# Kernel optimization log

Measured on AMD Instinct MI355X. Metric: run time of the kernel, lower is better.

The kernel has to match this reference:

```python
import jax, jax.numpy as jnp
import numpy as np

N_GRAPHS = 200
NODES_PER_GRAPH = 500
N_NODES = N_GRAPHS * NODES_PER_GRAPH  # 100000
N_EDGES = 1_600_000
INPUT_DIM = 64
GCN_DIM = 128
SEQ_LEN = 20
LSTM_DIM = 128
OUTPUT_DIM = 1


def setup_inputs() -> dict:
    key = jax.random.key(0)
    ks = jax.random.split(key, 10)
    # edges constrained to stay inside each graph (block-diagonal adjacency)
    src = jax.random.randint(ks[0], (N_EDGES,), 0, N_NODES, dtype=jnp.int32)
    dst_local = jax.random.randint(ks[1], (N_EDGES,), 0, NODES_PER_GRAPH, dtype=jnp.int32)
    dst = (src // NODES_PER_GRAPH) * NODES_PER_GRAPH + dst_local
    graph_ids = jnp.arange(N_NODES, dtype=jnp.int32) // NODES_PER_GRAPH
    x = jax.random.normal(ks[2], (N_NODES, INPUT_DIM), dtype=jnp.float32)
    s = 0.05
    w_gcn = jax.random.normal(ks[3], (INPUT_DIM, GCN_DIM), dtype=jnp.float32) * s
    b_gcn = jnp.zeros((GCN_DIM,), dtype=jnp.float32)
    w_ih = jax.random.normal(ks[4], (4 * LSTM_DIM, GCN_DIM), dtype=jnp.float32) * s
    w_hh = jax.random.normal(ks[5], (4 * LSTM_DIM, LSTM_DIM), dtype=jnp.float32) * s
    b_ih = jax.random.normal(ks[6], (4 * LSTM_DIM,), dtype=jnp.float32) * s
    b_hh = jax.random.normal(ks[7], (4 * LSTM_DIM,), dtype=jnp.float32) * s
    w_fc = jax.random.normal(ks[8], (OUTPUT_DIM, LSTM_DIM), dtype=jnp.float32) * s
    b_fc = jnp.zeros((OUTPUT_DIM,), dtype=jnp.float32)
    return {"x": x, "src": src, "dst": dst, "graph_ids": graph_ids,
            "w_gcn": w_gcn, "b_gcn": b_gcn, "w_ih": w_ih, "w_hh": w_hh,
            "b_ih": b_ih, "b_hh": b_hh, "w_fc": w_fc, "b_fc": b_fc}


def reference(x, src, dst, graph_ids, w_gcn, b_gcn, w_ih, w_hh, b_ih, b_hh, w_fc, b_fc):
    ones_e = jnp.ones((src.shape[0],), dtype=x.dtype)
    # DGL GraphConv norm='both': D_out^{-1/2} on src side, D_in^{-1/2} on dst side,
    # degrees clamped to min 1 (allow_zero_in_degree=True)
    out_deg = jnp.clip(jax.ops.segment_sum(ones_e, src, num_segments=N_NODES), 1.0)
    in_deg = jnp.clip(jax.ops.segment_sum(ones_e, dst, num_segments=N_NODES), 1.0)
    h = x * (out_deg ** -0.5)[:, None]                               # [N, Din]
    agg = jax.ops.segment_sum(h[src], dst, num_segments=N_NODES)     # gather+scatter-add
    h = agg * (in_deg ** -0.5)[:, None]
    h = jnp.maximum(h @ w_gcn + b_gcn, 0.0)                           # [N, GCN_DIM], ReLU
    # dgl.mean_nodes: per-graph mean pool
    cnt = jax.ops.segment_sum(jnp.ones((N_NODES,), h.dtype), graph_ids, num_segments=N_GRAPHS)
    hg = jax.ops.segment_sum(h, graph_ids, num_segments=N_GRAPHS) / cnt[:, None]  # [T, D]
    # build_dataset: sliding windows of length SEQ_LEN over the graph time series
    B = N_GRAPHS - SEQ_LEN + 1
    idx = jnp.arange(B)[:, None] + jnp.arange(SEQ_LEN)[None, :]
    dat = hg[idx]                                                      # [B, L, D]
    # single-layer LSTM (PyTorch gate order i,f,g,o), zero initial state
    x_proj = jnp.einsum('bld,gd->blg', dat, w_ih) + b_ih               # [B, L, 4H]
    h0 = jnp.zeros((B, LSTM_DIM), dat.dtype)
    c0 = jnp.zeros((B, LSTM_DIM), dat.dtype)

    def step(carry, xt):
        hprev, cprev = carry
        gates = xt + hprev @ w_hh.T + b_hh
        i, f, g, o = jnp.split(gates, 4, axis=-1)
        c = jax.nn.sigmoid(f) * cprev + jax.nn.sigmoid(i) * jnp.tanh(g)
        hh = jax.nn.sigmoid(o) * jnp.tanh(c)
        return (hh, c), None

    (h_n, _), _ = jax.lax.scan(step, (h0, c0), jnp.swapaxes(x_proj, 0, 1))
    pred = h_n @ w_fc.T + b_fc                                         # [B, OUTPUT_DIM]
    return pred
```

## Files before the change

### kernel.cpp

```cpp
#include <hip/hip_runtime.h>
#include <hip/hip_bf16.h>

#define N_GRAPHS 200
#define NPG      500
#define NPGP     512
#define N_NODES_ 100000
#define N_EDGES_ 1600000
#define DIN      64
#define DG       128
#define SEQ      20
#define HL       128
#define G4       512
#define BWIN     (N_GRAPHS - SEQ + 1)
#define NPART    256
#define EPB      (N_EDGES_/NPART)
#define SLOTS    64
#define CAP      9216

typedef __attribute__((ext_vector_type(8))) short short8;
typedef __attribute__((ext_vector_type(4))) float float4v;
typedef __attribute__((ext_vector_type(2))) _Float16 half2v;

__device__ __forceinline__ float sigmoidf_(float v){ return 1.0f/(1.0f+__expf(-v)); }
__device__ __forceinline__ float tanhf_(float x){
  float e = __expf(2.0f*x);
  return 1.0f - 2.0f/(e + 1.0f);
}

__device__ __forceinline__ unsigned short f2bf(float f) {
  unsigned int u = __float_as_uint(f);
  u += 0x7fffu + ((u >> 16) & 1u);
  return (unsigned short)(u >> 16);
}

__device__ __forceinline__ float h2dot(half2v a, half2v b, float c) {
#if __has_builtin(__builtin_amdgcn_fdot2)
  return __builtin_amdgcn_fdot2(a, b, c, false);
#else
  return c + (float)a.x*(float)b.x + (float)a.y*(float)b.y;
#endif
}

__global__ __launch_bounds__(1024) void k_part(const int* __restrict__ src,
                                               const int* __restrict__ dst,
                                               const float* __restrict__ w_hh,
                                               int* __restrict__ gcount,
                                               int* __restrict__ part,
                                               int4* __restrict__ whh16) {
  __shared__ int cnt[N_GRAPHS];
  __shared__ int base[N_GRAPHS];
  __shared__ int buf[N_GRAPHS][SLOTS];
  int b = blockIdx.x, t = threadIdx.x;
  if (b < 8) {
    int i = b*1024 + t;
    int k4 = i >> 9, r = i & 511;
    const float4* wp = (const float4*)(w_hh + (size_t)r*HL + k4*8);
    float4 w0 = wp[0], w1 = wp[1];
    half2v p0 = {(_Float16)w0.x, (_Float16)w0.y};
    half2v p1 = {(_Float16)w0.z, (_Float16)w0.w};
    half2v p2 = {(_Float16)w1.x, (_Float16)w1.y};
    half2v p3 = {(_Float16)w1.z, (_Float16)w1.w};
    int4 pk;
    pk.x = __builtin_bit_cast(int, p0); pk.y = __builtin_bit_cast(int, p1);
    pk.z = __builtin_bit_cast(int, p2); pk.w = __builtin_bit_cast(int, p3);
    whh16[i] = pk;
  }
  if (t < N_GRAPHS) cnt[t] = 0;
  __syncthreads();
  int e0 = b*EPB;
  const int2* s2 = (const int2*)(src + e0);
  const int2* d2 = (const int2*)(dst + e0);
  for (int i = t; i < EPB/2; i += 1024) {
    int2 ss = s2[i], dd = d2[i];
    {
      int g = ss.x / NPG;
      int pk = ((ss.x - g*NPG) << 9) | (dd.x - g*NPG);
      int pos = atomicAdd(&cnt[g], 1);
      if (pos < SLOTS) buf[g][pos] = pk;
      else { int gp = atomicAdd(&gcount[g], 1); part[g*CAP + gp] = pk; }
    }
    {
      int g = ss.y / NPG;
      int pk = ((ss.y - g*NPG) << 9) | (dd.y - g*NPG);
      int pos = atomicAdd(&cnt[g], 1);
      if (pos < SLOTS) buf[g][pos] = pk;
      else { int gp = atomicAdd(&gcount[g], 1); part[g*CAP + gp] = pk; }
    }
  }
  __syncthreads();
  if (t < N_GRAPHS) base[t] = atomicAdd(&gcount[t], min(cnt[t], SLOTS));
  __syncthreads();
  int w = t >> 6, lane = t & 63;
  for (int g = w; g < N_GRAPHS; g += 16) {
    int n = min(cnt[g], SLOTS);
    if (lane < n) part[g*CAP + base[g] + lane] = buf[g][lane];
  }
}

__global__ __launch_bounds__(1024) void k_graph(
    const int* __restrict__ gcount, const int* __restrict__ part,
    const float* __restrict__ x,
    const float* __restrict__ w_gcn, const float* __restrict__ b_gcn,
    const float* __restrict__ w_ih,  const float* __restrict__ b_ih,
    float* __restrict__ proj) {
  __shared__ int meta[2048];
  __shared__ int wsum[8];
  __shared__ int qhead;
  __shared__ __align__(16) float hgS[DG];
  __shared__ unsigned short sorted[CAP];
  __shared__ __align__(16) int4 xs[4008];
  __shared__ __align__(16) int4 hpre[4096];
  int* indeg  = meta;
  int* outdeg = meta + 512;
  int* off    = meta + 1024;
  float* soS  = (float*)(meta + 1536);
  int g = blockIdx.x, t = threadIdx.x;
  int lane = t & 63, w = t >> 6;

  float4 wg[2];
  #pragma unroll
  for (int q = 0; q < 2; ++q) wg[q] = ((const float4*)w_gcn)[t + q*1024];

  meta[t] = 0; meta[t + 1024] = 0;
  __syncthreads();
  int nseg = gcount[g], seg0 = g*CAP;
  int pr[9];
  #pragma unroll
  for (int q = 0; q < 9; ++q) {
    int e = t + q*1024;
    pr[q] = (e < nseg) ? part[seg0 + e] : -1;
  }
  #pragma unroll
  for (int q = 0; q < 9; ++q) {
    int p = pr[q];
    if (p >= 0) {
      atomicAdd(&indeg[p & 511], 1);
      atomicAdd(&outdeg[p >> 9], 1);
    }
  }
  __syncthreads();
  int vscan = 0, scscan = 0;
  if (t < 512) {
    vscan = indeg[t]; scscan = vscan;
    #pragma unroll
    for (int o = 1; o < 64; o <<= 1) { int nn = __shfl_up(scscan, o); if (lane >= o) scscan += nn; }
    if (lane == 63) wsum[w] = scscan;
  }
  __syncthreads();
  if (t < 512) {
    int woff = 0;
    #pragma unroll
    for (int i = 0; i < 8; ++i) woff += (i < w) ? wsum[i] : 0;
    off[t] = woff + scscan - vscan;
    soS[t] = rsqrtf((float)max(outdeg[t], 1));
  }
  __syncthreads();
  const float4* xg = ((const float4*)x) + (size_t)g*8000;
  ushort4* xd = (ushort4*)xs;
  for (int i = t; i < 8000; i += 1024) {
    float4 vv = xg[i];
    float s2 = soS[i >> 4];
    ushort4 u;
    u.x = f2bf(vv.x*s2); u.y = f2bf(vv.y*s2); u.z = f2bf(vv.z*s2); u.w = f2bf(vv.w*s2);
    xd[i] = u;
  }
  if (t < 16) xd[8000 + t] = make_ushort4(0,0,0,0);
  #pragma unroll
  for (int q = 0; q < 9; ++q) {
    int p = pr[q];
    if (p >= 0) {
      int pos = atomicAdd(&off[p & 511], 1);
      sorted[pos] = (unsigned short)(p >> 9);
    }
  }
  if (t == 0) qhead = 128;
  __syncthreads();
  int g8 = lane >> 3, fl = lane & 7;
  int nl = w*8 + g8;
  while (nl < 512) {
    int4 outv = make_int4(0,0,0,0);
    if (nl < NPG) {
      int end = off[nl], dgr = indeg[nl], st = end - dgr;
      float aHi[4] = {0.f,0.f,0.f,0.f};
      float aLo[4] = {0.f,0.f,0.f,0.f};
      int ev = (fl < dgr) ? (int)sorted[st + fl] : 500;
      for (int c0 = 0; c0 < dgr; c0 += 8) {
        int nc = c0 + 8;
        int evn = (nc + fl < dgr) ? (int)sorted[st + nc + fl] : 500;
        #pragma unroll
        for (int j = 0; j < 8; ++j) {
          int se = __shfl(ev, (g8 << 3) + j);
          int4 vv = xs[(se << 3) + fl];
          aHi[0] += __uint_as_float((unsigned)vv.x & 0xffff0000u);
          aLo[0] += __uint_as_float((unsigned)vv.x << 16);
          aHi[1] += __uint_as_float((unsigned)vv.y & 0xffff0000u);
          aLo[1] += __uint_as_float((unsigned)vv.y << 16);
          aHi[2] += __uint_as_float((unsigned)vv.z & 0xffff0000u);
          aLo[2] += __uint_as_float((unsigned)vv.z << 16);
          aHi[3] += __uint_as_float((unsigned)vv.w & 0xffff0000u);
          aLo[3] += __uint_as_float((unsigned)vv.w << 16);
        }
        ev = evn;
      }
      float sn = rsqrtf((float)max(dgr, 1));
      outv.x = (int)(((unsigned)f2bf(aLo[0]*sn)) | ((unsigned)f2bf(aHi[0]*sn) << 16));
      outv.y = (int)(((unsigned)f2bf(aLo[1]*sn)) | ((unsigned)f2bf(aHi[1]*sn) << 16));
      outv.z = (int)(((unsigned)f2bf(aLo[2]*sn)) | ((unsigned)f2bf(aHi[2]*sn) << 16));
      outv.w = (int)(((unsigned)f2bf(aLo[3]*sn)) | ((unsigned)f2bf(aHi[3]*sn) << 16));
    }
    hpre[(nl << 3) + (fl ^ (nl & 7))] = outv;
    int nxt = 0;
    if (fl == 0) nxt = atomicAdd(&qhead, 1);
    nl = __shfl(nxt, (g8 << 3));
  }
  __syncthreads();
  unsigned short* wLds = (unsigned short*)sorted;
  #pragma unroll
  for (int q = 0; q < 2; ++q) {
    int i = t + q*1024;
    int k = i >> 5, c4 = (i & 31) << 2;
    int h = k >> 5, j = k & 7, lhi = ((k >> 3) & 3) << 4;
    float vvv[4] = {wg[q].x, wg[q].y, wg[q].z, wg[q].w};
    #pragma unroll
    for (int u = 0; u < 4; ++u) {
      int n = c4 + u;
      int idx = ((n >> 4)*2 + h)*64 + lhi + (n & 15);
      wLds[idx*8 + j] = f2bf(vvv[u]);
    }
  }
  __syncthreads();
  float* pS = (float*)meta;
  int quad = lane >> 4, l15 = lane & 15;
  float bcol[8];
  #pragma unroll
  for (int nt = 0; nt < 8; ++nt) bcol[nt] = b_gcn[nt*16 + l15];
  float psum[8] = {0.f,0.f,0.f,0.f,0.f,0.f,0.f,0.f};
  #pragma unroll
  for (int i = 0; i < 2; ++i) {
    int row0 = (w + 16*i) << 4;
    int r = row0 + l15;
    int4 a0i = hpre[(r << 3) + (quad ^ (r & 7))];
    int4 a1i = hpre[(r << 3) + ((quad + 4) ^ (r & 7))];
    short8 a0 = *(const short8*)&a0i;
    short8 a1 = *(const short8*)&a1i;
    #pragma unroll
    for (int nt = 0; nt < 8; ++nt) {
      short8 b0 = *((const short8*)&wLds[((nt*2+0)*64 + lane)*8]);
      short8 b1 = *((const short8*)&wLds[((nt*2+1)*64 + lane)*8]);
      float4v acc = {0.f, 0.f, 0.f, 0.f};
      acc = __builtin_amdgcn_mfma_f32_16x16x32_bf16(a0, b0, acc, 0, 0, 0);
      acc = __builtin_amdgcn_mfma_f32_16x16x32_bf16(a1, b1, acc, 0, 0, 0);
      #pragma unroll
      for (int r4 = 0; r4 < 4; ++r4) {
        int node = row0 + quad*4 + r4;
        float vvv = acc[r4] + bcol[nt];
        psum[nt] += (node < NPG) ? fmaxf(vvv, 0.f) : 0.f;
      }
    }
  }
  #pragma unroll
  for (int nt = 0; nt < 8; ++nt) {
    float vvv = psum[nt];
    vvv += __shfl_xor(vvv, 16);
    vvv += __shfl_xor(vvv, 32);
    if (lane < 16) pS[w*DG + nt*16 + lane] = vvv;
  }
  __syncthreads();
  if (t < DG) {
    float sum = 0.f;
    #pragma unroll
    for (int w16 = 0; w16 < 16; ++w16) sum += pS[w16*DG + t];
    hgS[t] = sum * (1.0f/NPG);
  }
  __syncthreads();
  {
    int r = t >> 1, half = t & 1;
    const float4* wr = (const float4*)(w_ih + (size_t)r*HL) + half*16;
    const float4* hv = (const float4*)hgS + half*16;
    float acc = half ? 0.f : b_ih[r];
    #pragma unroll
    for (int k4 = 0; k4 < 16; ++k4) {
      float4 w4 = wr[k4]; float4 h4 = hv[k4];
      acc += w4.x*h4.x + w4.y*h4.y + w4.z*h4.z + w4.w*h4.w;
    }
    acc += __shfl_xor(acc, 1);
    if (!half) proj[(size_t)g*G4 + r] = acc;
  }
}

__global__ __launch_bounds__(512) void k_lstm(const float* __restrict__ proj,
    const int4* __restrict__ whh16, const float* __restrict__ b_hh,
    const float* __restrict__ w_fc, const float* __restrict__ b_fc,
    float* __restrict__ out) {
  __shared__ float gS[G4];
  __shared__ __align__(16) int4 hPi[16];
  __shared__ float fcS[2];
  int b = blockIdx.x, t = threadIdx.x;
  float pj[SEQ];
  #pragma unroll
  for (int l = 0; l < SEQ; ++l) pj[l] = proj[(size_t)(b+l)*G4 + t];
  int4 W[16];
  #pragma unroll
  for (int k4 = 0; k4 < 16; ++k4) W[k4] = whh16[(k4 << 9) + t];
  if (t < 16) hPi[t] = make_int4(0,0,0,0);
  float bh = b_hh[t];
  float c = 0.f;
  __syncthreads();
  #pragma unroll
  for (int l = 0; l < SEQ; ++l) {
    float a0 = pj[l] + bh;
    float a1 = 0.f, a2 = 0.f, a3 = 0.f;
    #pragma unroll
    for (int k4 = 0; k4 < 16; k4 += 4) {
      int4 hv0 = hPi[k4+0]; int4 hv1 = hPi[k4+1];
      int4 hv2 = hPi[k4+2]; int4 hv3 = hPi[k4+3];
      a0 = h2dot(__builtin_bit_cast(half2v, W[k4+0].x), __builtin_bit_cast(half2v, hv0.x), a0);
      a0 = h2dot(__builtin_bit_cast(half2v, W[k4+0].y), __builtin_bit_cast(half2v, hv0.y), a0);
      a0 = h2dot(__builtin_bit_cast(half2v, W[k4+0].z), __builtin_bit_cast(half2v, hv0.z), a0);
      a0 = h2dot(__builtin_bit_cast(half2v, W[k4+0].w), __builtin_bit_cast(half2v, hv0.w), a0);
      a1 = h2dot(__builtin_bit_cast(half2v, W[k4+1].x), __builtin_bit_cast(half2v, hv1.x), a1);
      a1 = h2dot(__builtin_bit_cast(half2v, W[k4+1].y), __builtin_bit_cast(half2v, hv1.y), a1);
      a1 = h2dot(__builtin_bit_cast(half2v, W[k4+1].z), __builtin_bit_cast(half2v, hv1.z), a1);
      a1 = h2dot(__builtin_bit_cast(half2v, W[k4+1].w), __builtin_bit_cast(half2v, hv1.w), a1);
      a2 = h2dot(__builtin_bit_cast(half2v, W[k4+2].x), __builtin_bit_cast(half2v, hv2.x), a2);
      a2 = h2dot(__builtin_bit_cast(half2v, W[k4+2].y), __builtin_bit_cast(half2v, hv2.y), a2);
      a2 = h2dot(__builtin_bit_cast(half2v, W[k4+2].z), __builtin_bit_cast(half2v, hv2.z), a2);
      a2 = h2dot(__builtin_bit_cast(half2v, W[k4+2].w), __builtin_bit_cast(half2v, hv2.w), a2);
      a3 = h2dot(__builtin_bit_cast(half2v, W[k4+3].x), __builtin_bit_cast(half2v, hv3.x), a3);
      a3 = h2dot(__builtin_bit_cast(half2v, W[k4+3].y), __builtin_bit_cast(half2v, hv3.y), a3);
      a3 = h2dot(__builtin_bit_cast(half2v, W[k4+3].z), __builtin_bit_cast(half2v, hv3.z), a3);
      a3 = h2dot(__builtin_bit_cast(half2v, W[k4+3].w), __builtin_bit_cast(half2v, hv3.w), a3);
    }
    gS[t] = (a0 + a1) + (a2 + a3);
    __syncthreads();
    if (t < 128) {
      float iv = sigmoidf_(gS[t]);
      float fv = sigmoidf_(gS[HL + t]);
      float gv = tanhf_(gS[2*HL + t]);
      float ov = sigmoidf_(gS[3*HL + t]);
      c = fv*c + iv*gv;
      float h = ov * tanhf_(c);
      float hp2 = __shfl_xor(h, 1);
      if (!(t & 1)) {
        half2v hp = {(_Float16)h, (_Float16)hp2};
        ((int*)hPi)[t >> 1] = __builtin_bit_cast(int, hp);
      }
      if (l == SEQ-1) {
        float s = h * w_fc[t];
        #pragma unroll
        for (int o = 32; o > 0; o >>= 1) s += __shfl_down(s, o);
        if ((t & 63) == 0) fcS[t >> 6] = s;
      }
    }
    __syncthreads();
  }
  if (t == 0) out[b] = fcS[0] + fcS[1] + b_fc[0];
}

extern "C" void kernel_launch(void* const* d_in, const int* in_sizes, int n_in,
                              void* d_out, int out_size, void* d_ws, size_t ws_size,
                              hipStream_t stream) {
  const float* x     = (const float*)d_in[0];
  const int*   src   = (const int*)d_in[1];
  const int*   dst   = (const int*)d_in[2];
  const float* w_gcn = (const float*)d_in[4];
  const float* b_gcn = (const float*)d_in[5];
  const float* w_ih  = (const float*)d_in[6];
  const float* w_hh  = (const float*)d_in[7];
  const float* b_ih  = (const float*)d_in[8];
  const float* b_hh  = (const float*)d_in[9];
  const float* w_fc  = (const float*)d_in[10];
  const float* b_fc  = (const float*)d_in[11];
  float* out = (float*)d_out;

  char* ws = (char*)d_ws;
  size_t off = 0;
  auto alloc = [&](size_t bytes) -> void* {
    void* p = ws + off; off += (bytes + 255) & ~(size_t)255; return p;
  };
  int* gcount  = (int*)alloc((size_t)N_GRAPHS*4);
  int* part    = (int*)alloc((size_t)N_GRAPHS*CAP*4);
  int4* whh16  = (int4*)alloc((size_t)8192*16);
  float* proj  = (float*)alloc((size_t)N_GRAPHS*G4*4);
  (void)ws_size; (void)in_sizes; (void)n_in; (void)out_size;

  hipMemsetAsync(gcount, 0, (size_t)N_GRAPHS*4, stream);
  k_part<<<NPART, 1024, 0, stream>>>(src, dst, w_hh, gcount, part, whh16);
  k_graph<<<N_GRAPHS, 1024, 0, stream>>>(gcount, part, x, w_gcn, b_gcn, w_ih, b_ih, proj);
  k_lstm<<<BWIN, 512, 0, stream>>>(proj, whh16, b_hh, w_fc, b_fc, out);
}
```

Measured before the change: 154.5 us.

## Use fixed per-block edge cells, padded neighbor lists, and a shuffle-based LSTM step

```diff
diff --git a/kernel.cpp b/kernel.cpp
--- a/kernel.cpp
+++ b/kernel.cpp
@@ -3,7 +3,6 @@
 
 #define N_GRAPHS 200
 #define NPG      500
-#define NPGP     512
 #define N_NODES_ 100000
 #define N_EDGES_ 1600000
 #define DIN      64
@@ -14,11 +13,13 @@
 #define BWIN     (N_GRAPHS - SEQ + 1)
 #define NPART    256
 #define EPB      (N_EDGES_/NPART)
-#define SLOTS    64
-#define CAP      9216
+#define CELL     80
+#define CPG      (NPART*CELL)
+#define SCAP     10752
 
 typedef __attribute__((ext_vector_type(8))) short short8;
 typedef __attribute__((ext_vector_type(4))) float float4v;
+typedef __attribute__((ext_vector_type(2))) float floatx2;
 typedef __attribute__((ext_vector_type(2))) _Float16 half2v;
 
 __device__ __forceinline__ float sigmoidf_(float v){ return 1.0f/(1.0f+__expf(-v)); }
@@ -44,12 +45,11 @@
 __global__ __launch_bounds__(1024) void k_part(const int* __restrict__ src,
                                                const int* __restrict__ dst,
                                                const float* __restrict__ w_hh,
-                                               int* __restrict__ gcount,
                                                int* __restrict__ part,
+                                               int* __restrict__ pcnt,
                                                int4* __restrict__ whh16) {
   __shared__ int cnt[N_GRAPHS];
-  __shared__ int base[N_GRAPHS];
-  __shared__ int buf[N_GRAPHS][SLOTS];
+  __shared__ int buf[N_GRAPHS][CELL];
   int b = blockIdx.x, t = threadIdx.x;
   if (b < 8) {
     int i = b*1024 + t;
@@ -76,72 +76,96 @@
       int g = ss.x / NPG;
       int pk = ((ss.x - g*NPG) << 9) | (dd.x - g*NPG);
       int pos = atomicAdd(&cnt[g], 1);
-      if (pos < SLOTS) buf[g][pos] = pk;
-      else { int gp = atomicAdd(&gcount[g], 1); part[g*CAP + gp] = pk; }
+      if (pos < CELL) buf[g][pos] = pk;
     }
     {
       int g = ss.y / NPG;
       int pk = ((ss.y - g*NPG) << 9) | (dd.y - g*NPG);
       int pos = atomicAdd(&cnt[g], 1);
-      if (pos < SLOTS) buf[g][pos] = pk;
-      else { int gp = atomicAdd(&gcount[g], 1); part[g*CAP + gp] = pk; }
-    }
-  }
-  __syncthreads();
-  if (t < N_GRAPHS) base[t] = atomicAdd(&gcount[t], min(cnt[t], SLOTS));
+      if (pos < CELL) buf[g][pos] = pk;
+    }
+  }
   __syncthreads();
   int w = t >> 6, lane = t & 63;
   for (int g = w; g < N_GRAPHS; g += 16) {
-    int n = min(cnt[g], SLOTS);
-    if (lane < n) part[g*CAP + base[g] + lane] = buf[g][lane];
-  }
+    int n = min(cnt[g], CELL);
+    int ba = g*CPG + b*CELL;
+    if (lane < n)      part[ba + lane]      = buf[g][lane];
+    if (lane + 64 < n) part[ba + lane + 64] = buf[g][lane + 64];
+  }
+  if (t < N_GRAPHS) pcnt[t*NPART + b] = min(cnt[t], CELL);
 }
 
 __global__ __launch_bounds__(1024) void k_graph(
-    const int* __restrict__ gcount, const int* __restrict__ part,
+    const int* __restrict__ pcnt, const int* __restrict__ part,
     const float* __restrict__ x,
     const float* __restrict__ w_gcn, const float* __restrict__ b_gcn,
     const float* __restrict__ w_ih,  const float* __restrict__ b_ih,
     float* __restrict__ proj) {
   __shared__ int meta[2048];
-  __shared__ int wsum[8];
-  __shared__ int qhead;
+  __shared__ int ccnt[256], coff[256];
+  __shared__ int wsum[8], wsum4[4];
+  __shared__ int qhead, nsegS;
   __shared__ __align__(16) float hgS[DG];
-  __shared__ unsigned short sorted[CAP];
+  __shared__ unsigned short sorted[SCAP];
   __shared__ __align__(16) int4 xs[4008];
   __shared__ __align__(16) int4 hpre[4096];
   int* indeg  = meta;
   int* outdeg = meta + 512;
   int* off    = meta + 1024;
   float* soS  = (float*)(meta + 1536);
+  int* eC     = (int*)xs;
   int g = blockIdx.x, t = threadIdx.x;
   int lane = t & 63, w = t >> 6;
 
+  const float4* xg = ((const float4*)x) + (size_t)g*8000;
+  float4 xr[8];
+  #pragma unroll
+  for (int q = 0; q < 8; ++q) {
+    int i = t + q*1024;
+    if (i < 8000) xr[q] = xg[i];
+  }
   float4 wg[2];
   #pragma unroll
   for (int q = 0; q < 2; ++q) wg[q] = ((const float4*)w_gcn)[t + q*1024];
 
   meta[t] = 0; meta[t + 1024] = 0;
-  __syncthreads();
-  int nseg = gcount[g], seg0 = g*CAP;
-  int pr[9];
-  #pragma unroll
-  for (int q = 0; q < 9; ++q) {
-    int e = t + q*1024;
-    pr[q] = (e < nseg) ? part[seg0 + e] : -1;
-  }
-  #pragma unroll
-  for (int q = 0; q < 9; ++q) {
-    int p = pr[q];
-    if (p >= 0) {
+  int cv = 0, csc = 0;
+  if (t < 256) {
+    cv = pcnt[g*NPART + t];
+    ccnt[t] = cv;
+    csc = cv;
+    #pragma unroll
+    for (int o = 1; o < 64; o <<= 1) { int nn = __shfl_up(csc, o); if (lane >= o) csc += nn; }
+    if (lane == 63) wsum4[w] = csc;
+  }
+  __syncthreads();
+  if (t < 256) {
+    int woff = 0;
+    #pragma unroll
+    for (int i = 0; i < 4; ++i) woff += (i < w) ? wsum4[i] : 0;
+    coff[t] = woff + csc - cv;
+    if (t == 255) nsegS = woff + csc;
+  }
+  __syncthreads();
+  #pragma unroll
+  for (int it = 0; it < 20; ++it) {
+    int slot = it*1024 + t;
+    unsigned cell = (unsigned)slot / CELL;
+    int k = slot - (int)cell*CELL;
+    if (k < ccnt[cell]) {
+      int p = part[(size_t)g*CPG + slot];
+      eC[coff[cell] + k] = p;
       atomicAdd(&indeg[p & 511], 1);
       atomicAdd(&outdeg[p >> 9], 1);
     }
   }
   __syncthreads();
-  int vscan = 0, scscan = 0;
+  int vscan = 0, v4 = 0, scscan = 0;
   if (t < 512) {
-    vscan = indeg[t]; scscan = vscan;
+    vscan = indeg[t];
+    v4 = (vscan + 3) & ~3;
+    scscan = v4;
     #pragma unroll
     for (int o = 1; o < 64; o <<= 1) { int nn = __shfl_up(scscan, o); if (lane >= o) scscan += nn; }
     if (lane == 63) wsum[w] = scscan;
@@ -151,29 +175,35 @@
     int woff = 0;
     #pragma unroll
     for (int i = 0; i < 8; ++i) woff += (i < w) ? wsum[i] : 0;
-    off[t] = woff + scscan - vscan;
+    off[t] = woff + scscan - v4;
     soS[t] = rsqrtf((float)max(outdeg[t], 1));
   }
-  __syncthreads();
-  const float4* xg = ((const float4*)x) + (size_t)g*8000;
+  if (t == 0) qhead = 128;
+  __syncthreads();
+  int nseg = nsegS;
+  for (int e = t; e < nseg; e += 1024) {
+    int p = eC[e];
+    int pos = atomicAdd(&off[p & 511], 1);
+    sorted[pos] = (unsigned short)(p >> 9);
+  }
+  __syncthreads();
+  if (t < 512) {
+    int e = off[t], ee = (e + 3) & ~3;
+    for (; e < ee; ++e) sorted[e] = 500;
+  }
   ushort4* xd = (ushort4*)xs;
-  for (int i = t; i < 8000; i += 1024) {
-    float4 vv = xg[i];
-    float s2 = soS[i >> 4];
-    ushort4 u;
-    u.x = f2bf(vv.x*s2); u.y = f2bf(vv.y*s2); u.z = f2bf(vv.z*s2); u.w = f2bf(vv.w*s2);
-    xd[i] = u;
+  #pragma unroll
+  for (int q = 0; q < 8; ++q) {
+    int i = t + q*1024;
+    if (i < 8000) {
+      float4 vv = xr[q];
+      float s2 = soS[i >> 4];
+      ushort4 u;
+      u.x = f2bf(vv.x*s2); u.y = f2bf(vv.y*s2); u.z = f2bf(vv.z*s2); u.w = f2bf(vv.w*s2);
+      xd[i] = u;
+    }
   }
   if (t < 16) xd[8000 + t] = make_ushort4(0,0,0,0);
-  #pragma unroll
-  for (int q = 0; q < 9; ++q) {
-    int p = pr[q];
-    if (p >= 0) {
-      int pos = atomicAdd(&off[p & 511], 1);
-      sorted[pos] = (unsigned short)(p >> 9);
-    }
-  }
-  if (t == 0) qhead = 128;
   __syncthreads();
   int g8 = lane >> 3, fl = lane & 7;
   int nl = w*8 + g8;
@@ -181,32 +211,29 @@
     int4 outv = make_int4(0,0,0,0);
     if (nl < NPG) {
       int end = off[nl], dgr = indeg[nl], st = end - dgr;
-      float aHi[4] = {0.f,0.f,0.f,0.f};
-      float aLo[4] = {0.f,0.f,0.f,0.f};
-      int ev = (fl < dgr) ? (int)sorted[st + fl] : 500;
-      for (int c0 = 0; c0 < dgr; c0 += 8) {
-        int nc = c0 + 8;
-        int evn = (nc + fl < dgr) ? (int)sorted[st + nc + fl] : 500;
+      floatx2 a0 = {0.f,0.f}, a1 = {0.f,0.f}, a2 = {0.f,0.f}, a3 = {0.f,0.f};
+      for (int c0 = 0; c0 < dgr; c0 += 4) {
+        ushort4 e4 = *(const ushort4*)(sorted + st + c0);
         #pragma unroll
-        for (int j = 0; j < 8; ++j) {
-          int se = __shfl(ev, (g8 << 3) + j);
+        for (int j = 0; j < 4; ++j) {
+          int se = (j==0) ? e4.x : (j==1) ? e4.y : (j==2) ? e4.z : e4.w;
           int4 vv = xs[(se << 3) + fl];
-          aHi[0] += __uint_as_float((unsigned)vv.x & 0xffff0000u);
-          aLo[0] += __uint_as_float((unsigned)vv.x << 16);
-          aHi[1] += __uint_as_float((unsigned)vv.y & 0xffff0000u);
-          aLo[1] += __uint_as_float((unsigned)vv.y << 16);
-          aHi[2] += __uint_as_float((unsigned)vv.z & 0xffff0000u);
-          aLo[2] += __uint_as_float((unsigned)vv.z << 16);
-          aHi[3] += __uint_as_float((unsigned)vv.w & 0xffff0000u);
-          aLo[3] += __uint_as_float((unsigned)vv.w << 16);
+          floatx2 u0 = { __uint_as_float((unsigned)vv.x & 0xffff0000u),
+                         __uint_as_float((unsigned)vv.x << 16) };
+          floatx2 u1 = { __uint_as_float((unsigned)vv.y & 0xffff0000u),
+                         __uint_as_float((unsigned)vv.y << 16) };
+          floatx2 u2 = { __uint_as_float((unsigned)vv.z & 0xffff0000u),
+                         __uint_as_float((unsigned)vv.z << 16) };
+          floatx2 u3 = { __uint_as_float((unsigned)vv.w & 0xffff0000u),
+                         __uint_as_float((unsigned)vv.w << 16) };
+          a0 += u0; a1 += u1; a2 += u2; a3 += u3;
         }
-        ev = evn;
       }
       float sn = rsqrtf((float)max(dgr, 1));
-      outv.x = (int)(((unsigned)f2bf(aLo[0]*sn)) | ((unsigned)f2bf(aHi[0]*sn) << 16));
-      outv.y = (int)(((unsigned)f2bf(aLo[1]*sn)) | ((unsigned)f2bf(aHi[1]*sn) << 16));
-      outv.z = (int)(((unsigned)f2bf(aLo[2]*sn)) | ((unsigned)f2bf(aHi[2]*sn) << 16));
-      outv.w = (int)(((unsigned)f2bf(aLo[3]*sn)) | ((unsigned)f2bf(aHi[3]*sn) << 16));
+      outv.x = (int)(((unsigned)f2bf(a0.y*sn)) | ((unsigned)f2bf(a0.x*sn) << 16));
+      outv.y = (int)(((unsigned)f2bf(a1.y*sn)) | ((unsigned)f2bf(a1.x*sn) << 16));
+      outv.z = (int)(((unsigned)f2bf(a2.y*sn)) | ((unsigned)f2bf(a2.x*sn) << 16));
+      outv.w = (int)(((unsigned)f2bf(a3.y*sn)) | ((unsigned)f2bf(a3.x*sn) << 16));
     }
     hpre[(nl << 3) + (fl ^ (nl & 7))] = outv;
     int nxt = 0;
@@ -292,28 +319,32 @@
     const int4* __restrict__ whh16, const float* __restrict__ b_hh,
     const float* __restrict__ w_fc, const float* __restrict__ b_fc,
     float* __restrict__ out) {
-  __shared__ float gS[G4];
-  __shared__ __align__(16) int4 hPi[16];
-  __shared__ float fcS[2];
+  __shared__ __align__(16) int4 hA[16], hB[16];
+  __shared__ float fcS[8];
   int b = blockIdx.x, t = threadIdx.x;
+  int e = t >> 2, q = t & 3;
+  int r = q*HL + e;
   float pj[SEQ];
   #pragma unroll
-  for (int l = 0; l < SEQ; ++l) pj[l] = proj[(size_t)(b+l)*G4 + t];
+  for (int l = 0; l < SEQ; ++l) pj[l] = proj[(size_t)(b+l)*G4 + r];
   int4 W[16];
   #pragma unroll
-  for (int k4 = 0; k4 < 16; ++k4) W[k4] = whh16[(k4 << 9) + t];
-  if (t < 16) hPi[t] = make_int4(0,0,0,0);
-  float bh = b_hh[t];
+  for (int k4 = 0; k4 < 16; ++k4) W[k4] = whh16[(k4 << 9) + r];
+  if (t < 16) hA[t] = make_int4(0,0,0,0);
+  float bh = b_hh[r];
+  float wfc = w_fc[e];
   float c = 0.f;
   __syncthreads();
   #pragma unroll
   for (int l = 0; l < SEQ; ++l) {
+    const int4* Rb = (l & 1) ? hB : hA;
+    int*       Wb = (int*)((l & 1) ? hA : hB);
     float a0 = pj[l] + bh;
     float a1 = 0.f, a2 = 0.f, a3 = 0.f;
     #pragma unroll
     for (int k4 = 0; k4 < 16; k4 += 4) {
-      int4 hv0 = hPi[k4+0]; int4 hv1 = hPi[k4+1];
-      int4 hv2 = hPi[k4+2]; int4 hv3 = hPi[k4+3];
+      int4 hv0 = Rb[k4+0]; int4 hv1 = Rb[k4+1];
+      int4 hv2 = Rb[k4+2]; int4 hv3 = Rb[k4+3];
       a0 = h2dot(__builtin_bit_cast(half2v, W[k4+0].x), __builtin_bit_cast(half2v, hv0.x), a0);
       a0 = h2dot(__builtin_bit_cast(half2v, W[k4+0].y), __builtin_bit_cast(half2v, hv0.y), a0);
       a0 = h2dot(__builtin_bit_cast(half2v, W[k4+0].z), __builtin_bit_cast(half2v, hv0.z), a0);
@@ -331,30 +362,38 @@
       a3 = h2dot(__builtin_bit_cast(half2v, W[k4+3].z), __builtin_bit_cast(half2v, hv3.z), a3);
       a3 = h2dot(__builtin_bit_cast(half2v, W[k4+3].w), __builtin_bit_cast(half2v, hv3.w), a3);
     }
-    gS[t] = (a0 + a1) + (a2 + a3);
+    float v = (a0 + a1) + (a2 + a3);
+    int base = t & ~3;
+    float iv = __shfl(v, base+0);
+    float fv = __shfl(v, base+1);
+    float gv = __shfl(v, base+2);
+    float ov = __shfl(v, base+3);
+    float h = 0.f;
+    if (q == 0) {
+      iv = sigmoidf_(iv); fv = sigmoidf_(fv);
+      gv = tanhf_(gv);    ov = sigmoidf_(ov);
+      c = fv*c + iv*gv;
+      h = ov * tanhf_(c);
+    }
+    float hRight = __shfl(h, (t & ~7) + 4);
+    if ((t & 7) == 0) {
+      half2v hp = {(_Float16)h, (_Float16)hRight};
+      Wb[e >> 1] = __builtin_bit_cast(int, hp);
+    }
+    if (l == SEQ-1) {
+      float s = (q == 0) ? h * wfc : 0.f;
+      #pragma unroll
+      for (int o = 32; o > 0; o >>= 1) s += __shfl_down(s, o);
+      if ((t & 63) == 0) fcS[t >> 6] = s;
+    }
     __syncthreads();
-    if (t < 128) {
-      float iv = sigmoidf_(gS[t]);
-      float fv = sigmoidf_(gS[HL + t]);
-      float gv = tanhf_(gS[2*HL + t]);
-      float ov = sigmoidf_(gS[3*HL + t]);
-      c = fv*c + iv*gv;
-      float h = ov * tanhf_(c);
-      float hp2 = __shfl_xor(h, 1);
-      if (!(t & 1)) {
-        half2v hp = {(_Float16)h, (_Float16)hp2};
-        ((int*)hPi)[t >> 1] = __builtin_bit_cast(int, hp);
-      }
-      if (l == SEQ-1) {
-        float s = h * w_fc[t];
-        #pragma unroll
-        for (int o = 32; o > 0; o >>= 1) s += __shfl_down(s, o);
-        if ((t & 63) == 0) fcS[t >> 6] = s;
-      }
-    }
-    __syncthreads();
-  }
-  if (t == 0) out[b] = fcS[0] + fcS[1] + b_fc[0];
+  }
+  if (t == 0) {
+    float s = 0.f;
+    #pragma unroll
+    for (int i = 0; i < 8; ++i) s += fcS[i];
+    out[b] = s + b_fc[0];
+  }
 }
 
 extern "C" void kernel_launch(void* const* d_in, const int* in_sizes, int n_in,
@@ -378,14 +417,13 @@
   auto alloc = [&](size_t bytes) -> void* {
     void* p = ws + off; off += (bytes + 255) & ~(size_t)255; return p;
   };
-  int* gcount  = (int*)alloc((size_t)N_GRAPHS*4);
-  int* part    = (int*)alloc((size_t)N_GRAPHS*CAP*4);
+  int* part    = (int*)alloc((size_t)N_GRAPHS*CPG*4);
+  int* pcnt    = (int*)alloc((size_t)N_GRAPHS*NPART*4);
   int4* whh16  = (int4*)alloc((size_t)8192*16);
   float* proj  = (float*)alloc((size_t)N_GRAPHS*G4*4);
   (void)ws_size; (void)in_sizes; (void)n_in; (void)out_size;
 
-  hipMemsetAsync(gcount, 0, (size_t)N_GRAPHS*4, stream);
-  k_part<<<NPART, 1024, 0, stream>>>(src, dst, w_hh, gcount, part, whh16);
-  k_graph<<<N_GRAPHS, 1024, 0, stream>>>(gcount, part, x, w_gcn, b_gcn, w_ih, b_ih, proj);
+  k_part<<<NPART, 1024, 0, stream>>>(src, dst, w_hh, part, pcnt, whh16);
+  k_graph<<<N_GRAPHS, 1024, 0, stream>>>(pcnt, part, x, w_gcn, b_gcn, w_ih, b_ih, proj);
   k_lstm<<<BWIN, 512, 0, stream>>>(proj, whh16, b_hh, w_fc, b_fc, out);
 }
```

After: 160.7 us. 4.0% more time.
